# Kernel tuning notes

Hardware: AMD Instinct MI355X
Metric: run time of the kernel (lower is better)

The kernel has to match this reference:

```python
import jax, jax.numpy as jnp
import numpy as np

# dims: batch, seq_len, d_model, heads, head_dim, n_buckets
B, L, DM, H, DH, K = 4, 4096, 1024, 16, 64, 8
C = L // K            # chunk length after bucket sort (512); extra_len==0 for these dims
CS = 0.1              # cluster_score mixing weight


def setup_inputs() -> dict:
    key = jax.random.key(0)
    ks = jax.random.split(key, 12)
    s = 0.02
    def p(k, shape):
        return jax.random.normal(k, shape, jnp.float32) * s
    return {
        "inputs_q": jax.random.normal(ks[0], (B, L, DM), jnp.float32),
        "wq": p(ks[1], (DM, H, DH)), "bq": jnp.zeros((H, DH), jnp.float32),
        "wk": p(ks[2], (DM, H, DH)), "bk": jnp.zeros((H, DH), jnp.float32),
        "wv": p(ks[3], (DM, H, DH)), "bv": jnp.zeros((H, DH), jnp.float32),
        "w_shared": p(ks[4], (H, DH, K)),
        "w_qscore": p(ks[5], (H, DH, K)),
        "w_kscore": p(ks[6], (H, DH, K)),
        "wo": p(ks[7], (H, DH, DM)), "bo": jnp.zeros((DM,), jnp.float32),
    }


def reference(inputs_q, wq, bq, wk, bk, wv, bv, w_shared, w_qscore, w_kscore, wo, bo):
    scale = 1.0 / np.sqrt(DH)
    # QKV projections (DenseGeneral to (H, DH))
    q = jnp.einsum('bld,dhk->blhk', inputs_q, wq) + bq  # [B,L,H,DH]
    k = jnp.einsum('bld,dhk->blhk', inputs_q, wk) + bk
    v = jnp.einsum('bld,dhk->blhk', inputs_q, wv) + bv

    # learned linear cluster scores on stop-gradient q/k
    mix_q = (1.0 - CS) * w_shared + CS * w_qscore  # [H,DH,K]
    mix_k = (1.0 - CS) * w_shared + CS * w_kscore
    qs = jnp.einsum('blhd,hdk->blhk', jax.lax.stop_gradient(q), mix_q)  # [B,L,H,K]
    ksc = jnp.einsum('blhd,hdk->blhk', jax.lax.stop_gradient(k), mix_k)

    # bucket assignment = argmax learned score; per-(batch,head) stable sort by bucket id
    bq_id = jnp.argmax(qs, -1).transpose(0, 2, 1)   # [B,H,L]
    bk_id = jnp.argmax(ksc, -1).transpose(0, 2, 1)
    sort_q = jnp.argsort(bq_id, axis=-1)            # stable in jax
    sort_k = jnp.argsort(bk_id, axis=-1)

    qh = q.transpose(0, 2, 1, 3)  # [B,H,L,DH]
    kh = k.transpose(0, 2, 1, 3)
    vh = v.transpose(0, 2, 1, 3)
    sq = jnp.take_along_axis(qh, sort_q[..., None], axis=2).reshape(B, H, K, C, DH)
    sk = jnp.take_along_axis(kh, sort_k[..., None], axis=2).reshape(B, H, K, C, DH)
    sv = jnp.take_along_axis(vh, sort_k[..., None], axis=2).reshape(B, H, K, C, DH)

    # block attention within each bucket chunk
    logits = jnp.einsum('bhncd,bhned->bhnce', sq, sk) * scale  # [B,H,K,C,C]
    attn = jax.nn.softmax(logits, axis=-1)
    o = jnp.einsum('bhnce,bhned->bhncd', attn, sv).reshape(B, H, L, DH)

    # unsort back to original token order
    inv_q = jnp.argsort(sort_q, axis=-1)
    o = jnp.take_along_axis(o, inv_q[..., None], axis=2)  # [B,H,L,DH]
    o = o.transpose(0, 2, 1, 3)                            # [B,L,H,DH]

    out = jnp.einsum('blhd,hdo->blo', o, wo) + bo          # output projection

    # auxiliary load-balancing routing loss over buckets (extra_loss)
    p_q = jax.nn.softmax(qs, -1)
    p_k = jax.nn.softmax(ksc, -1)
    f_q = jax.nn.one_hot(jnp.argmax(qs, -1), K, dtype=qs.dtype)
    f_k = jax.nn.one_hot(jnp.argmax(ksc, -1), K, dtype=qs.dtype)
    lq = K * jnp.mean(jnp.sum(jnp.mean(f_q, 1) * jnp.mean(p_q, 1), -1))
    lk = K * jnp.mean(jnp.sum(jnp.mean(f_k, 1) * jnp.mean(p_k, 1), -1))
    extra_loss = 0.5 * (lq + lk)
    return out, extra_loss
```

## Files before the change

kernel.cpp:

```cpp
#include <hip/hip_runtime.h>
#include <hip/hip_bf16.h>

#define BB 4
#define LL 4096
#define DM 1024
#define HH 16
#define DHD 64
#define KB 8
#define BL 16384
#define FLAGCAP 131072

typedef __attribute__((ext_vector_type(8))) short short8;
typedef __attribute__((ext_vector_type(4))) short short4v;
typedef __attribute__((ext_vector_type(4))) float float4v;

#define MFMA16(A, Bx, C) __builtin_amdgcn_mfma_f32_16x16x32_bf16(A, Bx, C, 0, 0, 0)

static __device__ __forceinline__ short bf16s(float f) {
  __hip_bfloat16 h = __float2bfloat16(f);
  return *reinterpret_cast<short*>(&h);
}
static __device__ __forceinline__ float b2f(short s) {
  __hip_bfloat16 h = *reinterpret_cast<__hip_bfloat16*>(&s);
  return __bfloat162float(h);
}
static __device__ __forceinline__ void gl16(const void* g, void* l) {
  __builtin_amdgcn_global_load_lds(
      (const __attribute__((address_space(1))) void*)g,
      (__attribute__((address_space(3))) void*)l, 16, 0, 0);
}

__global__ __launch_bounds__(256) void xcvt(const float* __restrict__ x,
                                            __hip_bfloat16* __restrict__ xb) {
  int i = (blockIdx.x * 256 + threadIdx.x) * 8;
  float4 f0 = *reinterpret_cast<const float4*>(x + i);
  float4 f1 = *reinterpret_cast<const float4*>(x + i + 4);
  short8 o;
  o[0] = bf16s(f0.x); o[1] = bf16s(f0.y); o[2] = bf16s(f0.z); o[3] = bf16s(f0.w);
  o[4] = bf16s(f1.x); o[5] = bf16s(f1.y); o[6] = bf16s(f1.z); o[7] = bf16s(f1.w);
  *reinterpret_cast<short8*>(xb + i) = o;
}

__global__ __launch_bounds__(256) void prep_wt(const float* __restrict__ wq,
                                               const float* __restrict__ wk,
                                               const float* __restrict__ wv,
                                               const float* __restrict__ wo,
                                               __hip_bfloat16* __restrict__ wt_qkv,
                                               __hip_bfloat16* __restrict__ wt_o) {
  int blk = blockIdx.x;
  int s = blk >> 8;
  int rem = blk & 255;
  int k0 = (rem >> 4) * 64;
  int n0 = (rem & 15) * 64;
  const float* src = (s == 0) ? wq : (s == 1) ? wk : (s == 2) ? wv : wo;
  __hip_bfloat16* dst = (s < 3) ? (wt_qkv + (size_t)s * 1024 * 1024) : wt_o;
  __shared__ float ls[64][65];
  int t = threadIdx.x;
#pragma unroll
  for (int p = 0; p < 4; ++p) {
    int sid = p * 256 + t;
    int r = sid >> 4, c4 = sid & 15;
    float4 v = *reinterpret_cast<const float4*>(src + (size_t)(k0 + r) * 1024 + n0 + c4 * 4);
    ls[r][c4 * 4 + 0] = v.x; ls[r][c4 * 4 + 1] = v.y;
    ls[r][c4 * 4 + 2] = v.z; ls[r][c4 * 4 + 3] = v.w;
  }
  __syncthreads();
#pragma unroll
  for (int p = 0; p < 4; ++p) {
    int sid = p * 256 + t;
    int n = sid >> 4, kq = sid & 15;
    short4v pk;
#pragma unroll
    for (int j = 0; j < 4; ++j) pk[j] = bf16s(ls[kq * 4 + j][n]);
    *reinterpret_cast<short4v*>(dst + (size_t)(n0 + n) * 1024 + k0 + kq * 4) = pk;
  }
}

__global__ __launch_bounds__(256) void prep_wsc(const float* __restrict__ wq,
                                                const float* __restrict__ wk,
                                                const float* __restrict__ wsh,
                                                const float* __restrict__ wqs,
                                                const float* __restrict__ wks,
                                                const float* __restrict__ bq,
                                                const float* __restrict__ bk,
                                                double* __restrict__ wscg,
                                                double* __restrict__ bsc,
                                                __hip_bfloat16* __restrict__ whb,
                                                __hip_bfloat16* __restrict__ wmb) {
  int col = blockIdx.x;
  int side = col >> 7, h = (col >> 3) & 15, kk = col & 7;
  int g = side * 16 + h;
  const float* w = side ? wk : wq;
  const float* wscore = side ? wks : wqs;
  __shared__ double mix[64];
  int t = threadIdx.x;
  if (t < 64)
    mix[t] = 0.9 * (double)wsh[(h * 64 + t) * 8 + kk] +
             0.1 * (double)wscore[(h * 64 + t) * 8 + kk];
  __syncthreads();
#pragma unroll
  for (int p = 0; p < 4; ++p) {
    int d = p * 256 + t;
    double acc = 0.0;
    const float* wr = w + (size_t)d * 1024 + h * 64;
#pragma unroll
    for (int j = 0; j < 64; ++j) acc += (double)wr[j] * mix[j];
    wscg[((size_t)g * 1024 + d) * 8 + kk] = acc;
    short hi = bf16s((float)acc);
    short mid = bf16s((float)(acc - (double)b2f(hi)));
    *reinterpret_cast<short*>(whb + (size_t)col * 1024 + d) = hi;
    *reinterpret_cast<short*>(wmb + (size_t)col * 1024 + d) = mid;
  }
  if (t == 0) {
    const float* br = (side ? bk : bq) + h * 64;
    double acc = 0.0;
    for (int j = 0; j < 64; ++j) acc += (double)br[j] * mix[j];
    bsc[col] = acc;
  }
}

__global__ __launch_bounds__(256) void score_gemm(const float* __restrict__ x,
                                                  const __hip_bfloat16* __restrict__ whb,
                                                  const __hip_bfloat16* __restrict__ wmb,
                                                  const double* __restrict__ bsc,
                                                  float* __restrict__ S2) {
  __shared__ char sm[49152];
  int t = threadIdx.x;
  int m0 = blockIdx.x * 64;
  int n0 = blockIdx.y * 128;
  int lane = t & 63;
  int wu = __builtin_amdgcn_readfirstlane(t >> 6);
  int lm = lane & 15, quad = lane >> 4;
  int wmr = (wu & 1) * 32, wn = (wu >> 1) * 64;
  int rb = wu * 32, rr = lane >> 3, phys = lane & 7;
  float4v zero = {0.f, 0.f, 0.f, 0.f};
  float4v acc[2][4];
#pragma unroll
  for (int i = 0; i < 2; ++i)
#pragma unroll
    for (int j = 0; j < 4; ++j) acc[i][j] = zero;

  for (int k0 = 0; k0 < 1024; k0 += 64) {
    __syncthreads();
#pragma unroll
    for (int p = 0; p < 2; ++p) {
      int sid = p * 256 + t;
      int m = sid >> 3, kc = sid & 7;
      const float* ap = x + (size_t)(m0 + m) * 1024 + k0 + kc * 8;
      float4 f0 = *reinterpret_cast<const float4*>(ap);
      float4 f1 = *reinterpret_cast<const float4*>(ap + 4);
      float vv[8] = {f0.x, f0.y, f0.z, f0.w, f1.x, f1.y, f1.z, f1.w};
      short8 hi, lo;
#pragma unroll
      for (int e = 0; e < 8; ++e) {
        short h = bf16s(vv[e]);
        hi[e] = h;
        lo[e] = bf16s(vv[e] - b2f(h));
      }
      *reinterpret_cast<short8*>(sm + m * 128 + ((kc + m) & 7) * 16) = hi;
      *reinterpret_cast<short8*>(sm + 8192 + m * 128 + ((kc + m) & 7) * 16) = lo;
    }
#pragma unroll
    for (int p = 0; p < 4; ++p) {
      int row = rb + p * 8 + rr;
      int kc = (phys - row) & 7;
      gl16(whb + (size_t)(n0 + row) * 1024 + k0 + kc * 8, sm + 16384 + (rb + p * 8) * 128);
      gl16(wmb + (size_t)(n0 + row) * 1024 + k0 + kc * 8, sm + 32768 + (rb + p * 8) * 128);
    }
    __syncthreads();
#pragma unroll
    for (int kh = 0; kh < 2; ++kh) {
      short8 ah[2], al[2], bh[4], bm[4];
#pragma unroll
      for (int i = 0; i < 2; ++i) {
        int row = wmr + i * 16 + lm;
        int ph = ((kh * 4 + quad) + row) & 7;
        ah[i] = *reinterpret_cast<const short8*>(sm + row * 128 + ph * 16);
        al[i] = *reinterpret_cast<const short8*>(sm + 8192 + row * 128 + ph * 16);
      }
#pragma unroll
      for (int j = 0; j < 4; ++j) {
        int rn = wn + j * 16 + lm;
        int ph = ((kh * 4 + quad) + rn) & 7;
        bh[j] = *reinterpret_cast<const short8*>(sm + 16384 + rn * 128 + ph * 16);
        bm[j] = *reinterpret_cast<const short8*>(sm + 32768 + rn * 128 + ph * 16);
      }
#pragma unroll
      for (int i = 0; i < 2; ++i)
#pragma unroll
        for (int j = 0; j < 4; ++j) {
          acc[i][j] = MFMA16(ah[i], bh[j], acc[i][j]);
          acc[i][j] = MFMA16(ah[i], bm[j], acc[i][j]);
          acc[i][j] = MFMA16(al[i], bh[j], acc[i][j]);
        }
    }
  }

#pragma unroll
  for (int i = 0; i < 2; ++i)
#pragma unroll
    for (int j = 0; j < 4; ++j) {
      int n = n0 + wn + j * 16 + lm;
      float bias = (float)bsc[n];
#pragma unroll
      for (int r = 0; r < 4; ++r) {
        int row = m0 + wmr + i * 16 + quad * 4 + r;
        S2[(size_t)(n >> 3) * 131072 + row * 8 + (n & 7)] = acc[i][j][r] + bias;
      }
    }
}

__global__ __launch_bounds__(512) void bucket_kernel(const float* __restrict__ S2,
                                                     int* __restrict__ bid,
                                                     float* __restrict__ psumg,
                                                     int* __restrict__ flagcnt,
                                                     int* __restrict__ list) {
  int t = threadIdx.x;
  int lane = t & 63;
  int w = t >> 6;
  int T0 = blockIdx.x * 64;
  int tg = T0 + lane;
  int b = tg >> 12, l = tg & 4095;
#pragma unroll
  for (int gi = 0; gi < 4; ++gi) {
    int g = gi * 8 + w;
    const float* sp = S2 + (size_t)g * 131072 + tg * 8;
    float4 v0 = *reinterpret_cast<const float4*>(sp);
    float4 v1 = *reinterpret_cast<const float4*>(sp + 4);
    float v[8] = {v0.x, v0.y, v0.z, v0.w, v1.x, v1.y, v1.z, v1.w};
    float mx = v[0]; int am = 0;
#pragma unroll
    for (int j = 1; j < 8; ++j) { if (v[j] > mx) { mx = v[j]; am = j; } }
    float mx2 = -3.0e38f;
#pragma unroll
    for (int j = 0; j < 8; ++j) { if (j != am && v[j] > mx2) mx2 = v[j]; }
    int side = g >> 4, h = g & 15;
    int slab = (side * 4 + b) * 16 + h;
    bid[(slab << 12) | l] = am;
    if (mx - mx2 < 5e-4f) {
      int pos = atomicAdd(flagcnt, 1);
      if (pos < FLAGCAP) list[pos] = (slab << 12) | l;
    }
    float es = 0.f, e[8];
#pragma unroll
    for (int j = 0; j < 8; ++j) { e[j] = __expf(v[j] - mx); es += e[j]; }
    float inv = 1.f / es;
#pragma unroll
    for (int j = 0; j < 8; ++j) {
      float s = e[j] * inv;
      s += __shfl_xor(s, 1);  s += __shfl_xor(s, 2);  s += __shfl_xor(s, 4);
      s += __shfl_xor(s, 8);  s += __shfl_xor(s, 16); s += __shfl_xor(s, 32);
      if (lane == 0) atomicAdd(&psumg[slab * 8 + j], s);
    }
  }
}

__global__ __launch_bounds__(256) void refine_kernel(const float* __restrict__ x,
                                                     const double* __restrict__ wscg,
                                                     const double* __restrict__ bsc,
                                                     const int* __restrict__ flagcnt,
                                                     const int* __restrict__ list,
                                                     int* __restrict__ bid) {
  int lane = threadIdx.x & 63;
  int w = threadIdx.x >> 6;
  int cnt = flagcnt[0];
  if (cnt > FLAGCAP) cnt = FLAGCAP;
  for (int i = blockIdx.x * 4 + w; i < cnt; i += 1024) {
    int e = list[i];
    int slab = e >> 12, l = e & 4095;
    int side = slab >> 6, b = (slab >> 4) & 3, h = slab & 15;
    int g = side * 16 + h;
    int row = b * 4096 + l;
    double acc[8] = {0, 0, 0, 0, 0, 0, 0, 0};
    const float* xr = x + (size_t)row * 1024 + lane * 16;
    const double* wr = wscg + ((size_t)g * 1024 + lane * 16) * 8;
#pragma unroll
    for (int dd = 0; dd < 16; ++dd) {
      double xv = (double)xr[dd];
#pragma unroll
      for (int j = 0; j < 8; ++j) acc[j] += xv * wr[dd * 8 + j];
    }
#pragma unroll
    for (int j = 0; j < 8; ++j) {
      double v = acc[j];
      v += __shfl_xor(v, 32); v += __shfl_xor(v, 16); v += __shfl_xor(v, 8);
      v += __shfl_xor(v, 4);  v += __shfl_xor(v, 2);  v += __shfl_xor(v, 1);
      acc[j] = v + bsc[g * 8 + j];
    }
    if (lane == 0) {
      double mx = acc[0]; int am = 0;
#pragma unroll
      for (int j = 1; j < 8; ++j) { if (acc[j] > mx) { mx = acc[j]; am = j; } }
      bid[(slab << 12) | l] = am;
    }
  }
}

__global__ __launch_bounds__(256) void sort_kernel(const int* __restrict__ bid,
                                                   int* __restrict__ sortq,
                                                   int* __restrict__ sortk,
                                                   int* __restrict__ cntg) {
  int blk = blockIdx.x;
  int side = blk >> 6, b = (blk >> 4) & 3, h = blk & 15;
  const int* ids = bid + (((side * 4 + b) * 16 + h) << 12);
  int* outp = (side ? sortk : sortq) + ((b * 16 + h) << 12);
  __shared__ int cnt[8][257];
  __shared__ int base[8];
  int t = threadIdx.x;
  int loc[16];
  int hist[8] = {0, 0, 0, 0, 0, 0, 0, 0};
#pragma unroll
  for (int j = 0; j < 16; ++j) { loc[j] = ids[t * 16 + j] & 7; hist[loc[j]]++; }
#pragma unroll
  for (int k = 0; k < 8; ++k) cnt[k][t + 1] = hist[k];
  if (t < 8) cnt[t][0] = 0;
  __syncthreads();
  if (t < 8) {
    for (int i = 1; i <= 256; ++i) cnt[t][i] += cnt[t][i - 1];
  }
  __syncthreads();
  if (t == 0) {
    int run = 0;
    for (int k = 0; k < 8; ++k) { base[k] = run; run += cnt[k][256]; }
  }
  if (t < 8) cntg[((side * 4 + b) * 16 + h) * 8 + t] = cnt[t][256];
  __syncthreads();
#pragma unroll
  for (int j = 0; j < 16; ++j) {
    int k = loc[j];
    int before = 0;
#pragma unroll
    for (int i = 0; i < 16; ++i) before += (i < j && loc[i] == k) ? 1 : 0;
    int pos = base[k] + cnt[k][t] + before;
    outp[pos] = t * 16 + j;
  }
}

template <bool CBF16>
__global__ __launch_bounds__(512, 2) void gemm256(const __hip_bfloat16* __restrict__ A,
                                                  const __hip_bfloat16* __restrict__ Bt,
                                                  void* __restrict__ Cv,
                                                  const float* __restrict__ b0,
                                                  const float* __restrict__ b1,
                                                  const float* __restrict__ b2,
                                                  int nblk) {
  __shared__ char sm[131072];
  int t = threadIdx.x;
  int blk = blockIdx.x;
  int m0 = (blk / nblk) * 256;
  int n0 = (blk % nblk) * 256;
  int lane = t & 63;
  int wu = __builtin_amdgcn_readfirstlane(t >> 6);
  int lm = lane & 15, quad = lane >> 4;
  int rr = lane >> 3, phys = lane & 7;
  int wrow = (wu & 1) * 64;
  int wcol = (wu >> 1) * 32;

  constexpr int QM[4] = {0, 0, 1, 1};
  constexpr int QN[4] = {0, 1, 1, 0};

  auto STAGE = [&](char* bufn, int j, int kS) {
    const int mat = (j == 1 || j == 2) ? 1 : 0;
    const int hm = (j >= 2) ? 1 : 0;
    const __hip_bfloat16* src = mat ? Bt : A;
    int gb = mat ? n0 : m0;
    char* lb = bufn + mat * 32768 + hm * 16384;
#pragma unroll
    for (int i = 0; i < 2; ++i) {
      int r = hm * 128 + (wu * 2 + i) * 8 + rr;
      int kc = (phys - r) & 7;
      gl16(src + (size_t)(gb + r) * 1024 + kS + kc * 8, lb + (wu * 2 + i) * 1024);
    }
  };

#pragma unroll
  for (int j = 0; j < 4; ++j) STAGE(sm, j, 0);

  float4v zero = {0.f, 0.f, 0.f, 0.f};
  float4v acc[4][4][2];
#pragma unroll
  for (int q = 0; q < 4; ++q)
#pragma unroll
    for (int mi = 0; mi < 4; ++mi)
#pragma unroll
      for (int ni = 0; ni < 2; ++ni) acc[q][mi][ni] = zero;

  short8 a[4][2], b[2][2];
  auto READA = [&](const char* bc, int qm) {
#pragma unroll
    for (int mi = 0; mi < 4; ++mi) {
      int row = qm * 128 + wrow + mi * 16 + lm;
#pragma unroll
      for (int ks = 0; ks < 2; ++ks) {
        int ph = ((ks * 4 + quad) + row) & 7;
        a[mi][ks] = *reinterpret_cast<const short8*>(bc + row * 128 + ph * 16);
      }
    }
  };
  auto READB = [&](const char* bc, int qn) {
#pragma unroll
    for (int ni = 0; ni < 2; ++ni) {
      int rn = qn * 128 + wcol + ni * 16 + lm;
#pragma unroll
      for (int ks = 0; ks < 2; ++ks) {
        int ph = ((ks * 4 + quad) + rn) & 7;
        b[ni][ks] = *reinterpret_cast<const short8*>(bc + 32768 + rn * 128 + ph * 16);
      }
    }
  };

#pragma unroll 1
  for (int kt = 0; kt < 16; ++kt) {
    char* bc = sm + ((kt & 1) << 16);
    char* bn = sm + (((kt & 1) ^ 1) << 16);
    int kS = (kt < 15) ? (kt + 1) * 64 : 960;
#pragma unroll
    for (int j = 0; j < 4; ++j) {
      if (j < 3) {
        asm volatile("s_waitcnt vmcnt(4)" ::: "memory");
        __builtin_amdgcn_s_barrier();
      }
      if (j == 0) { READA(bc, 0); READB(bc, 0); }
      else if (j == 1) { READB(bc, 1); }
      else if (j == 2) { READA(bc, 1); }
      else { READB(bc, 0); }
      STAGE(bn, j, kS);
      __builtin_amdgcn_s_setprio(1);
#pragma unroll
      for (int mi = 0; mi < 4; ++mi)
#pragma unroll
        for (int ni = 0; ni < 2; ++ni)
#pragma unroll
          for (int ks = 0; ks < 2; ++ks)
            acc[j][mi][ni] = MFMA16(a[mi][ks], b[ni][ks], acc[j][mi][ni]);
      __builtin_amdgcn_s_setprio(0);
    }
  }
  asm volatile("s_waitcnt vmcnt(0)" ::: "memory");

  if constexpr (CBF16) {
#pragma unroll
    for (int j = 0; j < 4; ++j)
#pragma unroll
      for (int mi = 0; mi < 4; ++mi)
#pragma unroll
        for (int ni = 0; ni < 2; ++ni) {
          int nn = n0 + QN[j] * 128 + wcol + ni * 16 + lm;
          int s = nn >> 10, nnb = nn & 1023;
          const float* bias = (s == 0) ? b0 : (s == 1) ? b1 : b2;
          float bvx = bias[nnb];
          __hip_bfloat16* C = (__hip_bfloat16*)Cv + (size_t)s * BL * 1024;
#pragma unroll
          for (int r = 0; r < 4; ++r) {
            int row = m0 + QM[j] * 128 + wrow + mi * 16 + quad * 4 + r;
            C[(size_t)row * 1024 + nnb] = __float2bfloat16(acc[j][mi][ni][r] + bvx);
          }
        }
  } else {
    float* C = (float*)Cv;
#pragma unroll
    for (int j = 0; j < 4; ++j)
#pragma unroll
      for (int mi = 0; mi < 4; ++mi)
#pragma unroll
        for (int ni = 0; ni < 2; ++ni) {
          int nn = n0 + QN[j] * 128 + wcol + ni * 16 + lm;
          float bvx = b0[nn];
#pragma unroll
          for (int r = 0; r < 4; ++r) {
            int row = m0 + QM[j] * 128 + wrow + mi * 16 + quad * 4 + r;
            C[(size_t)row * 1024 + nn] = acc[j][mi][ni][r] + bvx;
          }
        }
  }
}

__global__ __launch_bounds__(256) void vt_kernel(const __hip_bfloat16* __restrict__ vb,
                                                 const int* __restrict__ sortk,
                                                 __hip_bfloat16* __restrict__ vT) {
  int cid = blockIdx.x;
  int b = cid >> 7, h = (cid >> 3) & 15, n = cid & 7;
  int sbase = ((b * 16 + h) << 12) + n * 512;
  __shared__ __hip_bfloat16 ls[64][72];
  int t = threadIdx.x;
  for (int kt = 0; kt < 8; ++kt) {
    __syncthreads();
#pragma unroll
    for (int p = 0; p < 2; ++p) {
      int sid = p * 256 + t;
      int key = sid >> 3, kc = sid & 7;
      int tok = sortk[sbase + kt * 64 + key];
      short8 v = *reinterpret_cast<const short8*>(vb + ((size_t)(b * 4096 + tok) * 16 + h) * 64 + kc * 8);
      *reinterpret_cast<short8*>(&ls[key][kc * 8]) = v;
    }
    __syncthreads();
#pragma unroll
    for (int p = 0; p < 2; ++p) {
      int sid = p * 256 + t;
      int dim = sid >> 3, kc = sid & 7;
      short8 o;
#pragma unroll
      for (int j = 0; j < 8; ++j) o[j] = *reinterpret_cast<short*>(&ls[kc * 8 + j][dim]);
      *reinterpret_cast<short8*>(vT + ((size_t)cid * 64 + dim) * 512 + kt * 64 + kc * 8) = o;
    }
  }
}

__global__ __launch_bounds__(256) void attn_kernel(const __hip_bfloat16* __restrict__ qb,
                                                   const __hip_bfloat16* __restrict__ kb,
                                                   const __hip_bfloat16* __restrict__ vT,
                                                   const int* __restrict__ sortq,
                                                   const int* __restrict__ sortk,
                                                   __hip_bfloat16* __restrict__ ao) {
  __shared__ char sm[25600];
  int t = threadIdx.x;
  int lane = t & 63, w = t >> 6;
  int lm = lane & 15, quad = lane >> 4;
  int cid = blockIdx.x >> 3, qt = blockIdx.x & 7;
  int b = cid >> 7, h = (cid >> 3) & 15, n = cid & 7;
  int sbase = (b * 16 + h) << 12;
  int psOff = 16384 + w * 2304;

  int qtok = sortq[sbase + n * 512 + qt * 64 + w * 16 + lm];
  const __hip_bfloat16* qp = qb + ((size_t)(b * 4096 + qtok) * 16 + h) * 64 + quad * 8;
  short8 aq0 = *reinterpret_cast<const short8*>(qp);
  short8 aq1 = *reinterpret_cast<const short8*>(qp + 32);

  float4v zero = {0.f, 0.f, 0.f, 0.f};
  float4v accO[4];
#pragma unroll
  for (int i = 0; i < 4; ++i) accO[i] = zero;
  float lsum[4] = {0.f, 0.f, 0.f, 0.f};

  for (int kt = 0; kt < 8; ++kt) {
    __syncthreads();
#pragma unroll
    for (int p = 0; p < 2; ++p) {
      int sid = p * 256 + t;
      int row = sid >> 3, kc = sid & 7;
      int tok = sortk[sbase + n * 512 + kt * 64 + row];
      short8 kv = *reinterpret_cast<const short8*>(kb + ((size_t)(b * 4096 + tok) * 16 + h) * 64 + kc * 8);
      *reinterpret_cast<short8*>(sm + row * 128 + ((kc + row) & 7) * 16) = kv;
      short8 vv = *reinterpret_cast<const short8*>(vT + ((size_t)cid * 64 + row) * 512 + kt * 64 + kc * 8);
      *reinterpret_cast<short8*>(sm + 8192 + row * 128 + ((kc + row) & 7) * 16) = vv;
    }
    __syncthreads();
#pragma unroll
    for (int nt = 0; nt < 4; ++nt) {
      int key = nt * 16 + lm;
      int ph0 = (quad + key) & 7;
      int ph1 = (4 + quad + key) & 7;
      short8 bk0 = *reinterpret_cast<const short8*>(sm + key * 128 + ph0 * 16);
      short8 bk1 = *reinterpret_cast<const short8*>(sm + key * 128 + ph1 * 16);
      float4v S = zero;
      S = MFMA16(aq0, bk0, S);
      S = MFMA16(aq1, bk1, S);
#pragma unroll
      for (int r = 0; r < 4; ++r) {
        float e = __expf(S[r] * 0.125f);
        lsum[r] += e;
        *reinterpret_cast<short*>(sm + psOff + (quad * 4 + r) * 144 + key * 2) = bf16s(e);
      }
    }
    __builtin_amdgcn_s_waitcnt(0);
#pragma unroll
    for (int ks = 0; ks < 2; ++ks) {
      short8 ap = *reinterpret_cast<const short8*>(sm + psOff + lm * 144 + ks * 64 + quad * 16);
#pragma unroll
      for (int dt = 0; dt < 4; ++dt) {
        int dim = dt * 16 + lm;
        int ph = (ks * 4 + quad + dim) & 7;
        short8 bv = *reinterpret_cast<const short8*>(sm + 8192 + dim * 128 + ph * 16);
        accO[dt] = MFMA16(ap, bv, accO[dt]);
      }
    }
  }
#pragma unroll
  for (int r = 0; r < 4; ++r) {
    float l = lsum[r];
    l += __shfl_xor(l, 1); l += __shfl_xor(l, 2);
    l += __shfl_xor(l, 4); l += __shfl_xor(l, 8);
    lsum[r] = 1.f / l;
  }
#pragma unroll
  for (int dt = 0; dt < 4; ++dt)
#pragma unroll
    for (int r = 0; r < 4; ++r)
      *reinterpret_cast<short*>(sm + psOff + (quad * 4 + r) * 144 + (dt * 16 + lm) * 2) =
          bf16s(accO[dt][r] * lsum[r]);
  __builtin_amdgcn_s_waitcnt(0);
  int q2 = lane >> 2, c = lane & 3;
  int tok2 = sortq[sbase + n * 512 + qt * 64 + w * 16 + q2];
  __hip_bfloat16* op = ao + ((size_t)(b * 4096 + tok2) * 16 + h) * 64;
  short8 o0 = *reinterpret_cast<const short8*>(sm + psOff + q2 * 144 + c * 16);
  short8 o1 = *reinterpret_cast<const short8*>(sm + psOff + q2 * 144 + (c + 4) * 16);
  *reinterpret_cast<short8*>(op + c * 8) = o0;
  *reinterpret_cast<short8*>(op + (c + 4) * 8) = o1;
}

__global__ __launch_bounds__(1024) void loss_kernel(const int* __restrict__ cntg,
                                                    const float* __restrict__ psumg,
                                                    float* __restrict__ out) {
  int t = threadIdx.x;
  float term = ((float)cntg[t] * (1.f / 4096.f)) * (psumg[t] * (1.f / 4096.f));
#pragma unroll
  for (int o = 1; o < 64; o <<= 1) term += __shfl_xor(term, o);
  __shared__ float wsum[16];
  if ((t & 63) == 0) wsum[t >> 6] = term;
  __syncthreads();
  if (t == 0) {
    float s = 0.f;
    for (int i = 0; i < 16; ++i) s += wsum[i];
    out[16777216] = s * (1.f / 16.f);
  }
}

extern "C" void kernel_launch(void* const* d_in, const int* in_sizes, int n_in,
                              void* d_out, int out_size, void* d_ws, size_t ws_size,
                              hipStream_t stream) {
  (void)in_sizes; (void)n_in; (void)out_size; (void)ws_size;
  const float* x   = (const float*)d_in[0];
  const float* wq  = (const float*)d_in[1];
  const float* bq  = (const float*)d_in[2];
  const float* wk  = (const float*)d_in[3];
  const float* bk  = (const float*)d_in[4];
  const float* wv  = (const float*)d_in[5];
  const float* bv  = (const float*)d_in[6];
  const float* wsh = (const float*)d_in[7];
  const float* wqs = (const float*)d_in[8];
  const float* wks = (const float*)d_in[9];
  const float* wo  = (const float*)d_in[10];
  const float* bo  = (const float*)d_in[11];

  char* ws = (char*)d_ws;
  __hip_bfloat16* wt_qkv = (__hip_bfloat16*)(ws + 0);
  __hip_bfloat16* wt_o   = (__hip_bfloat16*)(ws + 6291456);
  double* wscg  = (double*)(ws + 8388608);
  double* bsc   = (double*)(ws + 10485760);
  __hip_bfloat16* qkv  = (__hip_bfloat16*)(ws + 10487808);
  __hip_bfloat16* whb = (__hip_bfloat16*)(ws + 109051904);
  __hip_bfloat16* wmb = (__hip_bfloat16*)(ws + 109576192);
  int* flagcnt = (int*)(ws + 110100480);
  int* list    = (int*)(ws + 110100736);
  __hip_bfloat16* attn = (__hip_bfloat16*)(ws + 111151104);
  float* S2 = (float*)(ws + 111151104);
  int* bid    = (int*)(ws + 144705536);
  int* sortq  = (int*)(ws + 146802688);
  int* sortk  = (int*)(ws + 147851264);
  float* psumg = (float*)(ws + 148899840);
  int* cntg    = (int*)(ws + 148903936);
  __hip_bfloat16* vT = (__hip_bfloat16*)d_out;
  __hip_bfloat16* xb = (__hip_bfloat16*)((char*)d_out + 33554432);
  float* out = (float*)d_out;

  hipMemsetAsync(psumg, 0, 8192, stream);
  hipMemsetAsync(flagcnt, 0, 4, stream);
  prep_wt<<<1024, 256, 0, stream>>>(wq, wk, wv, wo, wt_qkv, wt_o);
  prep_wsc<<<256, 256, 0, stream>>>(wq, wk, wsh, wqs, wks, bq, bk, wscg, bsc, whb, wmb);
  xcvt<<<8192, 256, 0, stream>>>(x, xb);
  score_gemm<<<dim3(256, 2), 256, 0, stream>>>(x, whb, wmb, bsc, S2);
  bucket_kernel<<<256, 512, 0, stream>>>(S2, bid, psumg, flagcnt, list);
  refine_kernel<<<256, 256, 0, stream>>>(x, wscg, bsc, flagcnt, list, bid);
  sort_kernel<<<128, 256, 0, stream>>>(bid, sortq, sortk, cntg);
  gemm256<true><<<768, 512, 0, stream>>>(xb, wt_qkv, qkv, bq, bk, bv, 12);
  vt_kernel<<<512, 256, 0, stream>>>(qkv + (size_t)2 * BL * 1024, sortk, vT);
  attn_kernel<<<4096, 256, 0, stream>>>(qkv, qkv + (size_t)BL * 1024, vT, sortq, sortk, attn);
  gemm256<false><<<256, 512, 0, stream>>>(attn, wt_o, (void*)out, bo, bo, bo, 4);
  loss_kernel<<<1, 1024, 0, stream>>>(cntg, psumg, out);
}
```

Before: 559.2 us.

## Keep both B fragments in registers and restructure GEMM phase barriers

The GEMM main loop now holds two B fragment sets in registers, so the fourth quadrant reuses B from the first instead of reading it again from LDS. The unrolled phase loop is replaced by explicit phases, each issuing its LDS reads and global staging, then a barrier and an lgkmcnt wait before the MFMA block. The aim is to cut LDS traffic and keep the staging loads in flight alongside the MFMAs. In exchange it adds extra barriers per k-step and raises register pressure, which could reduce occupancy.

```diff
diff --git a/kernel.cpp b/kernel.cpp
--- a/kernel.cpp
+++ b/kernel.cpp
@@ -385,7 +385,7 @@
 #pragma unroll
       for (int ni = 0; ni < 2; ++ni) acc[q][mi][ni] = zero;
 
-  short8 a[4][2], b[2][2];
+  short8 a[4][2], b0f[2][2], b1f[2][2];
   auto READA = [&](const char* bc, int qm) {
 #pragma unroll
     for (int mi = 0; mi < 4; ++mi) {
@@ -397,44 +397,63 @@
       }
     }
   };
-  auto READB = [&](const char* bc, int qn) {
+  auto READB = [&](short8 (&bb)[2][2], const char* bc, int qn) {
 #pragma unroll
     for (int ni = 0; ni < 2; ++ni) {
       int rn = qn * 128 + wcol + ni * 16 + lm;
 #pragma unroll
       for (int ks = 0; ks < 2; ++ks) {
         int ph = ((ks * 4 + quad) + rn) & 7;
-        b[ni][ks] = *reinterpret_cast<const short8*>(bc + 32768 + rn * 128 + ph * 16);
+        bb[ni][ks] = *reinterpret_cast<const short8*>(bc + 32768 + rn * 128 + ph * 16);
       }
     }
   };
+
+#define PH_MFMA(J, BB)                                                      \
+  __builtin_amdgcn_s_setprio(1);                                            \
+  _Pragma("unroll") for (int mi = 0; mi < 4; ++mi)                          \
+      _Pragma("unroll") for (int ni = 0; ni < 2; ++ni)                      \
+          _Pragma("unroll") for (int ks = 0; ks < 2; ++ks)                  \
+              acc[J][mi][ni] = MFMA16(a[mi][ks], BB[ni][ks], acc[J][mi][ni]); \
+  __builtin_amdgcn_s_setprio(0);
+
+  asm volatile("s_waitcnt vmcnt(4)" ::: "memory");
+  __builtin_amdgcn_s_barrier();
 
 #pragma unroll 1
   for (int kt = 0; kt < 16; ++kt) {
     char* bc = sm + ((kt & 1) << 16);
     char* bn = sm + (((kt & 1) ^ 1) << 16);
     int kS = (kt < 15) ? (kt + 1) * 64 : 960;
-#pragma unroll
-    for (int j = 0; j < 4; ++j) {
-      if (j < 3) {
-        asm volatile("s_waitcnt vmcnt(4)" ::: "memory");
-        __builtin_amdgcn_s_barrier();
-      }
-      if (j == 0) { READA(bc, 0); READB(bc, 0); }
-      else if (j == 1) { READB(bc, 1); }
-      else if (j == 2) { READA(bc, 1); }
-      else { READB(bc, 0); }
-      STAGE(bn, j, kS);
-      __builtin_amdgcn_s_setprio(1);
-#pragma unroll
-      for (int mi = 0; mi < 4; ++mi)
-#pragma unroll
-        for (int ni = 0; ni < 2; ++ni)
-#pragma unroll
-          for (int ks = 0; ks < 2; ++ks)
-            acc[j][mi][ni] = MFMA16(a[mi][ks], b[ni][ks], acc[j][mi][ni]);
-      __builtin_amdgcn_s_setprio(0);
-    }
+
+    READA(bc, 0); READB(b0f, bc, 0);
+    STAGE(bn, 0, kS);
+    __builtin_amdgcn_s_barrier();
+    asm volatile("s_waitcnt lgkmcnt(0)" ::: "memory");
+    PH_MFMA(0, b0f)
+    asm volatile("s_waitcnt vmcnt(4)" ::: "memory");
+    __builtin_amdgcn_s_barrier();
+
+    READB(b1f, bc, 1);
+    STAGE(bn, 1, kS);
+    __builtin_amdgcn_s_barrier();
+    asm volatile("s_waitcnt lgkmcnt(0)" ::: "memory");
+    PH_MFMA(1, b1f)
+    asm volatile("s_waitcnt vmcnt(4)" ::: "memory");
+    __builtin_amdgcn_s_barrier();
+
+    READA(bc, 1);
+    STAGE(bn, 2, kS);
+    __builtin_amdgcn_s_barrier();
+    asm volatile("s_waitcnt lgkmcnt(0)" ::: "memory");
+    PH_MFMA(2, b1f)
+    __builtin_amdgcn_s_barrier();
+
+    STAGE(bn, 3, kS);
+    __builtin_amdgcn_s_barrier();
+    PH_MFMA(3, b0f)
+    asm volatile("s_waitcnt vmcnt(4)" ::: "memory");
+    __builtin_amdgcn_s_barrier();
   }
   asm volatile("s_waitcnt vmcnt(0)" ::: "memory");
 
@@ -473,6 +492,7 @@
           }
         }
   }
+#undef PH_MFMA
 }
 
 __global__ __launch_bounds__(256) void vt_kernel(const __hip_bfloat16* __restrict__ vb,
```

New measurement: 550.4 us. No clear change (-1.6%).
